# Performance work log

Measured on AMD Instinct MI355X. Metric: run time of the kernel, lower is better.

The kernel has to match this reference:

```python
import jax, jax.numpy as jnp
import numpy as np

N = 100000   # nodes
E = 1600000  # edges (avg degree 16)
D = 128      # in_channels == hidden_channels
H = 4        # heads
C = D // H   # per-head channels = 32


def leaky(x, slope):
    return jnp.where(x >= 0, x, slope * x)


def setup_inputs() -> dict:
    key = jax.random.key(0)
    ks = jax.random.split(key, 12)
    s = 1.0 / np.sqrt(D)
    return {
        "x": jax.random.normal(ks[0], (N, D), jnp.float32),
        "edge_index": jax.random.randint(ks[1], (2, E), 0, N, jnp.int32),
        "edge_type": jax.random.randint(ks[2], (E,), 0, 8, jnp.int32),
        # linear1 (first_layer=True): LeakyReLU(0.01) -> Linear(D, D)
        "W1": jax.random.normal(ks[3], (D, D), jnp.float32) * s,
        "b1": jnp.zeros((D,), jnp.float32),
        # GATConv params: lin (no bias), att_src/att_dst [1,H,C], output bias [H*C]
        "Wg": jax.random.normal(ks[4], (D, D), jnp.float32) * s,
        "att_src": jax.random.normal(ks[5], (1, H, C), jnp.float32) * s,
        "att_dst": jax.random.normal(ks[6], (1, H, C), jnp.float32) * s,
        "bias_g": jnp.zeros((D,), jnp.float32),
        # linear2: LeakyReLU(0.01) -> Linear(D, D)
        "W2": jax.random.normal(ks[7], (D, D), jnp.float32) * s,
        "b2": jnp.zeros((D,), jnp.float32),
    }


def reference(x, edge_index, edge_type, W1, b1, Wg, att_src, att_dst, bias_g, W2, b2):
    # dropout layers act in eval mode (identity); edge_type is unused by forward.
    # linear1: LeakyReLU(0.01) then Linear
    x = leaky(x, 0.01) @ W1.T + b1                      # [N, D]

    # GATConv (add_self_loops=False, concat heads)
    h = (x @ Wg.T).reshape(N, H, C)                     # [N, H, C]
    a_src = jnp.sum(h * att_src, axis=-1)               # [N, H]
    a_dst = jnp.sum(h * att_dst, axis=-1)               # [N, H]

    src, dst = edge_index[0], edge_index[1]
    alpha = leaky(a_src[src] + a_dst[dst], 0.2)          # [E, H]

    # segment softmax over destination nodes (numerically stable)
    amax = jax.ops.segment_max(alpha, dst, num_segments=N)   # [N, H], -inf for empty
    amax = jnp.where(jnp.isfinite(amax), amax, 0.0)
    ex = jnp.exp(alpha - amax[dst])                      # [E, H]
    denom = jax.ops.segment_sum(ex, dst, num_segments=N) # [N, H]
    coeff = ex / (denom[dst] + 1e-16)                    # [E, H]

    msg = h[src] * coeff[:, :, None]                     # [E, H, C]
    out = jax.ops.segment_sum(msg, dst, num_segments=N)  # [N, H, C]
    out = out.reshape(N, H * C) + bias_g                 # [N, D]

    # linear2: LeakyReLU(0.01) then Linear; Dropout(0.3) identity at eval
    out = leaky(out, 0.01) @ W2.T + b2                   # [N, D]
    return out
```

## Files before the change

### kernel.cpp

```cpp
#include <hip/hip_runtime.h>
#include <hip/hip_bf16.h>

#define D128 128

typedef __attribute__((ext_vector_type(8))) short bf16x8;
typedef __attribute__((ext_vector_type(4))) float f32x4;

__device__ __forceinline__ float b2f(unsigned short u) {
    union { unsigned int i; float f; } z;
    z.i = ((unsigned int)u) << 16;
    return z.f;
}

__device__ __forceinline__ unsigned short f2b(float f) {
    union { float f; unsigned int i; } z;
    z.f = f;
    unsigned int r = z.i + 0x7FFFu + ((z.i >> 16) & 1u);
    return (unsigned short)(r >> 16);
}

__device__ __forceinline__ f32x4 mfma16(bf16x8 a, bf16x8 b, f32x4 c) {
    return __builtin_amdgcn_mfma_f32_16x16x32_bf16(a, b, c, 0, 0, 0);
}

#define CHUNK 8192
#define MAXBINS 512
#define BINCAP 8192
#define NGB 768
#define NFB 768

__global__ __launch_bounds__(256) void k_prep1(
    const float* __restrict__ W1, const float* __restrict__ Wg,
    const float* __restrict__ b1,
    const int* __restrict__ ei, int* __restrict__ M,
    float* __restrict__ Wc, float* __restrict__ bc,
    int E, int B, int nbins)
{
    __shared__ float wgr[256];
    __shared__ int hist[MAXBINS];
    const int t = threadIdx.x;
    if (blockIdx.x < 64) {
        const int i0 = blockIdx.x * 2;
        wgr[t] = Wg[i0 * 128 + t];
        __syncthreads();
        const int half = t >> 7;
        const int j = t & 127;
        const float* wr = &wgr[half * 128];
        float acc = 0.f;
        #pragma unroll 4
        for (int k = 0; k < 128; ++k)
            acc += wr[k] * W1[k * 128 + j];
        Wc[(i0 + half) * 128 + j] = acc;
        if (j == 0) {
            float ab = 0.f;
            for (int k = 0; k < 128; ++k) ab += wr[k] * b1[k];
            bc[i0 + half] = ab;
        }
    } else {
        const int chunk = blockIdx.x - 64;
        for (int i = t; i < nbins; i += 256) hist[i] = 0;
        __syncthreads();
        const int base = chunk * CHUNK;
        const int end = min(base + CHUNK, E);
        for (int e = base + t; e < end; e += 256)
            atomicAdd(&hist[ei[E + e] >> 8], 1);
        __syncthreads();
        for (int i = t; i < nbins; i += 256)
            M[i * B + chunk] = hist[i];
    }
}

__global__ __launch_bounds__(256) void k_prep2s(
    const float* __restrict__ Wc, const float* __restrict__ bc,
    const float* __restrict__ att_s, const float* __restrict__ att_d,
    const float* __restrict__ W2,
    unsigned short* __restrict__ Wcat, unsigned short* __restrict__ W2l,
    float* __restrict__ lbias,
    const int* __restrict__ M, int* __restrict__ scanned,
    int* __restrict__ bsum, int nM)
{
    __shared__ int lds[256];
    const int b = blockIdx.x, t = threadIdx.x;
    if (b < 9) {
        const int q = b * 256 + t;
        const int ct = q >> 8, rem = q & 255;
        const int ks = rem >> 6, lane = rem & 63;
        const int ldiv = lane >> 4, lmod = lane & 15;
        const int kb = ks * 32 + ldiv * 8;
        float v[8];
        if (ct < 8) {
            const int rho = ct * 16 + lmod;
            const float4 a = *(const float4*)(Wc + rho * 128 + kb);
            const float4 bq = *(const float4*)(Wc + rho * 128 + kb + 4);
            v[0] = a.x; v[1] = a.y; v[2] = a.z; v[3] = a.w;
            v[4] = bq.x; v[5] = bq.y; v[6] = bq.z; v[7] = bq.w;
        } else {
            #pragma unroll
            for (int e = 0; e < 8; ++e) v[e] = 0.f;
            if (lmod < 8) {
                const int hh = lmod & 3;
                const float* av = lmod < 4 ? att_s : att_d;
                for (int c = 0; c < 32; ++c) {
                    const float w = av[hh * 32 + c];
                    const float* wrow = Wc + (hh * 32 + c) * 128 + kb;
                    #pragma unroll
                    for (int e = 0; e < 8; ++e) v[e] += w * wrow[e];
                }
            }
        }
        union { uint4 qq; unsigned short s[8]; } o;
        #pragma unroll
        for (int e = 0; e < 8; ++e) o.s[e] = f2b(v[e]);
        *(uint4*)(Wcat + q * 8) = o.qq;
    } else if (b < 17) {
        const int q = (b - 9) * 256 + t;
        const int ct = q >> 8, rem = q & 255;
        const int ks = rem >> 6, lane = rem & 63;
        const int ldiv = lane >> 4, lmod = lane & 15;
        const int kb = ks * 32 + ldiv * 8;
        const int rho = ct * 16 + lmod;
        const float4 a = *(const float4*)(W2 + rho * 128 + kb);
        const float4 bq = *(const float4*)(W2 + rho * 128 + kb + 4);
        union { uint4 qq; unsigned short s[8]; } o;
        o.s[0] = f2b(a.x); o.s[1] = f2b(a.y); o.s[2] = f2b(a.z); o.s[3] = f2b(a.w);
        o.s[4] = f2b(bq.x); o.s[5] = f2b(bq.y); o.s[6] = f2b(bq.z); o.s[7] = f2b(bq.w);
        *(uint4*)(W2l + q * 8) = o.qq;
    } else if (b == 17) {
        if (t < 144) {
            float v = 0.f;
            if (t < 128) v = bc[t];
            else if (t < 136) {
                const int hh = (t - 128) & 3;
                const float* av = t < 132 ? att_s : att_d;
                for (int c = 0; c < 32; ++c) v += av[hh * 32 + c] * bc[hh * 32 + c];
            }
            lbias[t] = v;
        }
    } else {
        const int sid = b - 18;
        const int g0 = sid * 1024 + t * 4;
        int v0 = g0     < nM ? M[g0]     : 0;
        int v1 = g0 + 1 < nM ? M[g0 + 1] : 0;
        int v2 = g0 + 2 < nM ? M[g0 + 2] : 0;
        int v3 = g0 + 3 < nM ? M[g0 + 3] : 0;
        const int s = v0 + v1 + v2 + v3;
        lds[t] = s;
        __syncthreads();
        #pragma unroll
        for (int off = 1; off < 256; off <<= 1) {
            int tv = t >= off ? lds[t - off] : 0;
            __syncthreads();
            lds[t] += tv;
            __syncthreads();
        }
        int run = lds[t] - s;
        if (g0     < nM) scanned[g0]     = run;
        run += v0;
        if (g0 + 1 < nM) scanned[g0 + 1] = run;
        run += v1;
        if (g0 + 2 < nM) scanned[g0 + 2] = run;
        run += v2;
        if (g0 + 3 < nM) scanned[g0 + 3] = run;
        if (t == 255) bsum[sid] = lds[255];
    }
}

__global__ __launch_bounds__(256) void k_gemmA2(
    const float* __restrict__ x,
    const unsigned short* __restrict__ Wcat,
    const float* __restrict__ lbias,
    unsigned short* __restrict__ hfeat,
    float* __restrict__ asrc, float* __restrict__ adst,
    const int* __restrict__ ei, const int* __restrict__ scanned,
    const int* __restrict__ bsum, unsigned int* __restrict__ binned,
    int N, int E, int B, int nbins, int nM, int ntiles)
{
    __shared__ __align__(16) unsigned char smem[36864];
    const int t = threadIdx.x;
    if (blockIdx.x >= B) {
        unsigned short* sW = (unsigned short*)smem;
        const int wave = t >> 6, lane = t & 63, lmod = lane & 15, ldiv = lane >> 4;

        #pragma unroll
        for (int r = 0; r < 9; ++r)
            *(uint4*)&sW[r * 2048 + t * 8] = *(const uint4*)(Wcat + r * 2048 + t * 8);
        __syncthreads();

        for (int tile = blockIdx.x - B; tile < ntiles; tile += NGB) {
            const int rowBase = tile * 64;
            int row = rowBase + wave * 16 + lmod;
            row = min(row, N - 1);
            bf16x8 afr[4];
            #pragma unroll
            for (int ks = 0; ks < 4; ++ks) {
                const float* px = x + (size_t)row * D128 + ks * 32 + ldiv * 8;
                float4 f0 = *(const float4*)px;
                float4 f1 = *(const float4*)(px + 4);
                float tmp[8] = { f0.x, f0.y, f0.z, f0.w, f1.x, f1.y, f1.z, f1.w };
                union { bf16x8 v; unsigned short s[8]; } o;
                #pragma unroll
                for (int jj = 0; jj < 8; ++jj) {
                    float f = tmp[jj];
                    f = f >= 0.f ? f : 0.01f * f;
                    o.s[jj] = f2b(f);
                }
                afr[ks] = o.v;
            }

            f32x4 acc[9] = {};
            #pragma unroll
            for (int ct = 0; ct < 9; ++ct) {
                #pragma unroll
                for (int ks = 0; ks < 4; ++ks) {
                    bf16x8 bfr = *(const bf16x8*)&sW[(ct * 256 + ks * 64 + lane) * 8];
                    acc[ct] = mfma16(afr[ks], bfr, acc[ct]);
                }
            }

            const int orow = rowBase + wave * 16 + ldiv * 4;
            #pragma unroll
            for (int ct = 0; ct < 8; ++ct) {
                const int col = ct * 16 + lmod;
                const float bias = lbias[col];
                #pragma unroll
                for (int r = 0; r < 4; ++r)
                    if (orow + r < N)
                        hfeat[(size_t)(orow + r) * D128 + col] = f2b(acc[ct][r] + bias);
            }
            if (lmod < 8) {
                const float lb = lbias[128 + lmod];
                float* dst = lmod < 4 ? asrc : adst;
                const int hh = lmod & 3;
                #pragma unroll
                for (int r = 0; r < 4; ++r)
                    if (orow + r < N)
                        dst[(size_t)(orow + r) * 4 + hh] = acc[8][r] + lb;
            }
        }
    } else {
        int* cursor = (int*)smem;
        int* bpre   = (int*)(smem + MAXBINS * 4);
        const int chunk = blockIdx.x;
        const int nsb = (nM + 1023) >> 10;
        for (int i = t; i < nsb; i += 256) bpre[i] = bsum[i];
        __syncthreads();
        if (t == 0) {
            int run = 0;
            for (int i = 0; i < nsb; ++i) { int tv = bpre[i]; bpre[i] = run; run += tv; }
        }
        __syncthreads();
        for (int i = t; i < nbins; i += 256) {
            const int idx = i * B + chunk;
            cursor[i] = scanned[idx] + bpre[idx >> 10];
        }
        __syncthreads();
        const int base = chunk * CHUNK;
        const int end = min(base + CHUNK, E);
        for (int e = base + t; e < end; e += 256) {
            const int s = ei[e], d = ei[E + e];
            const int pos = atomicAdd(&cursor[d >> 8], 1);
            binned[pos] = ((unsigned int)(d & 255) << 20) | (unsigned int)s;
        }
    }
}

__global__ __launch_bounds__(256) void kB(
    const unsigned int* __restrict__ binned, const int* __restrict__ scanned,
    const int* __restrict__ bsum, int* __restrict__ bucket,
    int* __restrict__ rowstart, int* __restrict__ rowend,
    int E, int B, int nbins, int N, int nM)
{
    __shared__ unsigned int eb[BINCAP];
    __shared__ int ldeg[256];
    __shared__ int lscan[256];
    __shared__ int lcur[256];
    __shared__ int bpre[1024];
    const int nsb = (nM + 1023) >> 10;
    for (int i = threadIdx.x; i < nsb; i += 256) bpre[i] = bsum[i];
    __syncthreads();
    if (threadIdx.x == 0) {
        int run = 0;
        for (int i = 0; i < nsb; ++i) { int tv = bpre[i]; bpre[i] = run; run += tv; }
    }
    __syncthreads();
    const int bin = blockIdx.x;
    const int i0 = bin * B;
    const int binstart = scanned[i0] + bpre[i0 >> 10];
    int binend;
    if (bin + 1 < nbins) {
        const int i1 = (bin + 1) * B;
        binend = scanned[i1] + bpre[i1 >> 10];
    } else {
        binend = E;
    }
    int n = binend - binstart;
    if (n > BINCAP) n = BINCAP;

    for (int i = threadIdx.x; i < n; i += 256) eb[i] = binned[binstart + i];
    ldeg[threadIdx.x] = 0;
    __syncthreads();
    for (int i = threadIdx.x; i < n; i += 256)
        atomicAdd(&ldeg[eb[i] >> 20], 1);
    __syncthreads();
    const int v = ldeg[threadIdx.x];
    lscan[threadIdx.x] = v;
    __syncthreads();
    #pragma unroll
    for (int off = 1; off < 256; off <<= 1) {
        int tv = threadIdx.x >= off ? lscan[threadIdx.x - off] : 0;
        __syncthreads();
        lscan[threadIdx.x] += tv;
        __syncthreads();
    }
    const int excl = lscan[threadIdx.x] - v;
    lcur[threadIdx.x] = excl;
    const int d = (bin << 8) + threadIdx.x;
    if (d < N) {
        rowstart[d] = binstart + excl;
        rowend[d]   = binstart + excl + v;
    }
    __syncthreads();
    for (int i = threadIdx.x; i < n; i += 256) {
        const unsigned int p = eb[i];
        const int lp = atomicAdd(&lcur[p >> 20], 1);
        bucket[binstart + lp] = (int)(p & 0xFFFFFu);
    }
}

__global__ __launch_bounds__(256) void k_gat(
    const int* __restrict__ bucket,
    const int* __restrict__ rowstart, const int* __restrict__ rowend,
    const float* __restrict__ asrc, const float* __restrict__ adst,
    const unsigned short* __restrict__ hfeat,
    const float* __restrict__ bias_g,
    unsigned short* __restrict__ outbf, int N)
{
    const int wave = threadIdx.x >> 6;
    const int lane = threadIdx.x & 63;
    const int g    = lane >> 4;
    const int gl   = lane & 15;
    const int h    = gl >> 2;
    const int d    = blockIdx.x * 16 + wave * 4 + g;

    int start = 0, end = 0;
    float a_d = 0.f;
    if (d < N) {
        start = rowstart[d];
        end   = rowend[d];
        a_d   = adst[(size_t)d * 4 + h];
    }
    const unsigned int chb = (unsigned int)(gl << 3);
    const unsigned short* hbase = hfeat + chb;

    float acc[8] = {0.f, 0.f, 0.f, 0.f, 0.f, 0.f, 0.f, 0.f};
    float denom = 0.f;

    int j = start;
    for (; j + 2 <= end; j += 2) {
        const int s0 = bucket[j];
        const int s1 = bucket[j + 1];
        const float as0 = asrc[((size_t)s0 << 2) + h];
        const float as1 = asrc[((size_t)s1 << 2) + h];
        const uint4 hp0 = *(const uint4*)(hbase + ((unsigned int)s0 << 7));
        const uint4 hp1 = *(const uint4*)(hbase + ((unsigned int)s1 << 7));
        float a0 = as0 + a_d; a0 = a0 >= 0.f ? a0 : 0.2f * a0;
        float a1 = as1 + a_d; a1 = a1 >= 0.f ? a1 : 0.2f * a1;
        const float w0 = __expf(a0), w1 = __expf(a1);
        denom += w0 + w1;
        acc[0] += w0 * b2f((unsigned short)(hp0.x & 0xFFFFu)) + w1 * b2f((unsigned short)(hp1.x & 0xFFFFu));
        acc[1] += w0 * b2f((unsigned short)(hp0.x >> 16))     + w1 * b2f((unsigned short)(hp1.x >> 16));
        acc[2] += w0 * b2f((unsigned short)(hp0.y & 0xFFFFu)) + w1 * b2f((unsigned short)(hp1.y & 0xFFFFu));
        acc[3] += w0 * b2f((unsigned short)(hp0.y >> 16))     + w1 * b2f((unsigned short)(hp1.y >> 16));
        acc[4] += w0 * b2f((unsigned short)(hp0.z & 0xFFFFu)) + w1 * b2f((unsigned short)(hp1.z & 0xFFFFu));
        acc[5] += w0 * b2f((unsigned short)(hp0.z >> 16))     + w1 * b2f((unsigned short)(hp1.z >> 16));
        acc[6] += w0 * b2f((unsigned short)(hp0.w & 0xFFFFu)) + w1 * b2f((unsigned short)(hp1.w & 0xFFFFu));
        acc[7] += w0 * b2f((unsigned short)(hp0.w >> 16))     + w1 * b2f((unsigned short)(hp1.w >> 16));
    }
    if (j < end) {
        const int s0 = bucket[j];
        const float as0 = asrc[((size_t)s0 << 2) + h];
        const uint4 hp0 = *(const uint4*)(hbase + ((unsigned int)s0 << 7));
        float a0 = as0 + a_d; a0 = a0 >= 0.f ? a0 : 0.2f * a0;
        const float w0 = __expf(a0);
        denom += w0;
        acc[0] += w0 * b2f((unsigned short)(hp0.x & 0xFFFFu));
        acc[1] += w0 * b2f((unsigned short)(hp0.x >> 16));
        acc[2] += w0 * b2f((unsigned short)(hp0.y & 0xFFFFu));
        acc[3] += w0 * b2f((unsigned short)(hp0.y >> 16));
        acc[4] += w0 * b2f((unsigned short)(hp0.z & 0xFFFFu));
        acc[5] += w0 * b2f((unsigned short)(hp0.z >> 16));
        acc[6] += w0 * b2f((unsigned short)(hp0.w & 0xFFFFu));
        acc[7] += w0 * b2f((unsigned short)(hp0.w >> 16));
    }

    if (d < N) {
        const float inv = 1.f / (denom + 1e-16f);
        const float4 bg0 = *(const float4*)(bias_g + chb);
        const float4 bg1 = *(const float4*)(bias_g + chb + 4);
        const float bg[8] = { bg0.x, bg0.y, bg0.z, bg0.w, bg1.x, bg1.y, bg1.z, bg1.w };
        unsigned short s[8];
        #pragma unroll
        for (int k2 = 0; k2 < 8; ++k2) {
            float v = acc[k2] * inv + bg[k2];
            v = v >= 0.f ? v : 0.01f * v;
            s[k2] = f2b(v);
        }
        uint4 o;
        o.x = ((unsigned int)s[1] << 16) | s[0];
        o.y = ((unsigned int)s[3] << 16) | s[2];
        o.z = ((unsigned int)s[5] << 16) | s[4];
        o.w = ((unsigned int)s[7] << 16) | s[6];
        *(uint4*)(outbf + (((unsigned int)d << 7) + chb)) = o;
    }
}

__global__ __launch_bounds__(256) void k_final(
    const unsigned short* __restrict__ gatbf,
    const unsigned short* __restrict__ W2l,
    const float* __restrict__ b2,
    float* __restrict__ out, int N, int ntiles)
{
    __shared__ __align__(16) unsigned short sW[16384];
    const int t = threadIdx.x;
    const int wave = t >> 6, lane = t & 63, lmod = lane & 15, ldiv = lane >> 4;

    #pragma unroll
    for (int r = 0; r < 8; ++r)
        *(uint4*)&sW[r * 2048 + t * 8] = *(const uint4*)(W2l + r * 2048 + t * 8);
    __syncthreads();

    for (int tile = blockIdx.x; tile < ntiles; tile += NFB) {
        const int rowBase = tile * 64;
        int row = rowBase + wave * 16 + lmod;
        row = min(row, N - 1);
        bf16x8 afr[4];
        #pragma unroll
        for (int ks = 0; ks < 4; ++ks)
            afr[ks] = *(const bf16x8*)(gatbf + (size_t)row * D128 + ks * 32 + ldiv * 8);

        f32x4 acc[8] = {};
        #pragma unroll
        for (int ct = 0; ct < 8; ++ct) {
            #pragma unroll
            for (int ks = 0; ks < 4; ++ks) {
                bf16x8 bfr = *(const bf16x8*)&sW[(ct * 256 + ks * 64 + lane) * 8];
                acc[ct] = mfma16(afr[ks], bfr, acc[ct]);
            }
        }

        const int orow = rowBase + wave * 16 + ldiv * 4;
        #pragma unroll
        for (int ct = 0; ct < 8; ++ct) {
            const int col = ct * 16 + lmod;
            const float bb = b2[col];
            #pragma unroll
            for (int r = 0; r < 4; ++r)
                if (orow + r < N)
                    out[(size_t)(orow + r) * D128 + col] = acc[ct][r] + bb;
        }
    }
}

extern "C" void kernel_launch(void* const* d_in, const int* in_sizes, int n_in,
                              void* d_out, int out_size, void* d_ws, size_t ws_size,
                              hipStream_t stream)
{
    const float* x    = (const float*)d_in[0];
    const int*   ei   = (const int*)d_in[1];
    const float* W1   = (const float*)d_in[3];
    const float* b1   = (const float*)d_in[4];
    const float* Wg   = (const float*)d_in[5];
    const float* atts = (const float*)d_in[6];
    const float* attd = (const float*)d_in[7];
    const float* bg   = (const float*)d_in[8];
    const float* W2   = (const float*)d_in[9];
    const float* b2   = (const float*)d_in[10];
    float* out = (float*)d_out;

    const int N = in_sizes[0] / D128;
    const int E = in_sizes[1] / 2;

    const int B     = (E + CHUNK - 1) / CHUNK;
    const int nbins = (N + 255) >> 8;
    const int nM    = nbins * B;
    const int nsb   = (nM + 1023) / 1024;
    const int ntiles = (N + 63) / 64;

    char* ws = (char*)d_ws;
    float* Wc = (float*)ws;
    size_t off = 65536;
    float* bc    = (float*)(ws + off); off += 512;
    float* lbias = (float*)(ws + off); off += 1024;
    unsigned short* Wcat = (unsigned short*)(ws + off); off += 36864;
    unsigned short* W2l  = (unsigned short*)(ws + off); off += 32768;
    unsigned short* hfeat = (unsigned short*)(ws + off); off += (size_t)N * D128 * 2;
    float* asrc = (float*)(ws + off); off += (size_t)N * 4 * 4;
    float* adst = (float*)(ws + off); off += (size_t)N * 4 * 4;
    int* M       = (int*)(ws + off); off += (size_t)nM * 4;
    int* scanned = (int*)(ws + off); off += (size_t)nM * 4;
    int* bsum    = (int*)(ws + off); off += 1024 * 4;
    unsigned int* binned = (unsigned int*)(ws + off); off += (size_t)E * 4;
    int* bucket  = (int*)(ws + off); off += (size_t)E * 4;
    int* rowstart = (int*)(ws + off); off += (size_t)N * 4;
    int* rowend   = (int*)(ws + off); off += (size_t)N * 4;
    unsigned short* outbf = (unsigned short*)(ws + off); off += (size_t)N * D128 * 2;

    k_prep1<<<64 + B, 256, 0, stream>>>(W1, Wg, b1, ei, M, Wc, bc, E, B, nbins);
    k_prep2s<<<18 + nsb, 256, 0, stream>>>(Wc, bc, atts, attd, W2, Wcat, W2l,
                                           lbias, M, scanned, bsum, nM);
    k_gemmA2<<<B + NGB, 256, 0, stream>>>(x, Wcat, lbias, hfeat, asrc, adst,
                                          ei, scanned, bsum, binned,
                                          N, E, B, nbins, nM, ntiles);
    kB<<<nbins, 256, 0, stream>>>(binned, scanned, bsum, bucket,
                                  rowstart, rowend, E, B, nbins, N, nM);
    k_gat<<<(N + 15) / 16, 256, 0, stream>>>(bucket, rowstart, rowend,
                                             asrc, adst, hfeat, bg, outbf, N);
    k_final<<<NFB, 256, 0, stream>>>(outbf, W2l, b2, out, N, ntiles);
}
```

Measured before the change: 275.3 us.

## Replace global scan-based edge binning with atomic fixed-capacity bins and fewer launches

```diff
diff --git a/kernel.cpp b/kernel.cpp
--- a/kernel.cpp
+++ b/kernel.cpp
@@ -23,25 +23,43 @@
     return __builtin_amdgcn_mfma_f32_16x16x32_bf16(a, b, c, 0, 0, 0);
 }
 
-#define CHUNK 8192
-#define MAXBINS 512
-#define BINCAP 8192
+#define CHUNK2 4096
+#define BINW   128
+#define BINCAP 4096
+#define MAXBINS 1024
 #define NGB 768
 #define NFB 768
 
-__global__ __launch_bounds__(256) void k_prep1(
+__global__ __launch_bounds__(256) void k_prep(
     const float* __restrict__ W1, const float* __restrict__ Wg,
     const float* __restrict__ b1,
-    const int* __restrict__ ei, int* __restrict__ M,
-    float* __restrict__ Wc, float* __restrict__ bc,
+    const float* __restrict__ att_s, const float* __restrict__ att_d,
+    const float* __restrict__ W2,
+    const int* __restrict__ ei,
+    unsigned short* __restrict__ Wcat, unsigned short* __restrict__ W2l,
+    float* __restrict__ lbias,
+    unsigned int* __restrict__ binned, int* __restrict__ binFill,
     int E, int B, int nbins)
 {
-    __shared__ float wgr[256];
-    __shared__ int hist[MAXBINS];
     const int t = threadIdx.x;
-    if (blockIdx.x < 64) {
-        const int i0 = blockIdx.x * 2;
-        wgr[t] = Wg[i0 * 128 + t];
+    const int b = blockIdx.x;
+    if (b < 68) {
+        __shared__ float wgr[256];
+        __shared__ float rowout[2][128];
+        if (b < 64) {
+            const int i0 = b * 2;
+            wgr[t] = Wg[i0 * 128 + t];
+        } else {
+            const int q = (b - 64) * 2 + (t >> 7);
+            const int h = q & 3;
+            const float* av = q < 4 ? att_s : att_d;
+            const int k = t & 127;
+            float v = 0.f;
+            #pragma unroll 8
+            for (int c = 0; c < 32; ++c)
+                v += av[h * 32 + c] * Wg[(h * 32 + c) * 128 + k];
+            wgr[t] = v;
+        }
         __syncthreads();
         const int half = t >> 7;
         const int j = t & 127;
@@ -50,70 +68,29 @@
         #pragma unroll 4
         for (int k = 0; k < 128; ++k)
             acc += wr[k] * W1[k * 128 + j];
-        Wc[(i0 + half) * 128 + j] = acc;
+        rowout[half][j] = acc;
         if (j == 0) {
             float ab = 0.f;
             for (int k = 0; k < 128; ++k) ab += wr[k] * b1[k];
-            bc[i0 + half] = ab;
-        }
-    } else {
-        const int chunk = blockIdx.x - 64;
-        for (int i = t; i < nbins; i += 256) hist[i] = 0;
-        __syncthreads();
-        const int base = chunk * CHUNK;
-        const int end = min(base + CHUNK, E);
-        for (int e = base + t; e < end; e += 256)
-            atomicAdd(&hist[ei[E + e] >> 8], 1);
-        __syncthreads();
-        for (int i = t; i < nbins; i += 256)
-            M[i * B + chunk] = hist[i];
-    }
-}
-
-__global__ __launch_bounds__(256) void k_prep2s(
-    const float* __restrict__ Wc, const float* __restrict__ bc,
-    const float* __restrict__ att_s, const float* __restrict__ att_d,
-    const float* __restrict__ W2,
-    unsigned short* __restrict__ Wcat, unsigned short* __restrict__ W2l,
-    float* __restrict__ lbias,
-    const int* __restrict__ M, int* __restrict__ scanned,
-    int* __restrict__ bsum, int nM)
-{
-    __shared__ int lds[256];
-    const int b = blockIdx.x, t = threadIdx.x;
-    if (b < 9) {
-        const int q = b * 256 + t;
-        const int ct = q >> 8, rem = q & 255;
-        const int ks = rem >> 6, lane = rem & 63;
-        const int ldiv = lane >> 4, lmod = lane & 15;
-        const int kb = ks * 32 + ldiv * 8;
-        float v[8];
-        if (ct < 8) {
-            const int rho = ct * 16 + lmod;
-            const float4 a = *(const float4*)(Wc + rho * 128 + kb);
-            const float4 bq = *(const float4*)(Wc + rho * 128 + kb + 4);
-            v[0] = a.x; v[1] = a.y; v[2] = a.z; v[3] = a.w;
-            v[4] = bq.x; v[5] = bq.y; v[6] = bq.z; v[7] = bq.w;
-        } else {
-            #pragma unroll
-            for (int e = 0; e < 8; ++e) v[e] = 0.f;
-            if (lmod < 8) {
-                const int hh = lmod & 3;
-                const float* av = lmod < 4 ? att_s : att_d;
-                for (int c = 0; c < 32; ++c) {
-                    const float w = av[hh * 32 + c];
-                    const float* wrow = Wc + (hh * 32 + c) * 128 + kb;
-                    #pragma unroll
-                    for (int e = 0; e < 8; ++e) v[e] += w * wrow[e];
-                }
-            }
-        }
-        union { uint4 qq; unsigned short s[8]; } o;
-        #pragma unroll
-        for (int e = 0; e < 8; ++e) o.s[e] = f2b(v[e]);
-        *(uint4*)(Wcat + q * 8) = o.qq;
-    } else if (b < 17) {
-        const int q = (b - 9) * 256 + t;
+            const int rho = (b < 64) ? b * 2 + half : 128 + (b - 64) * 2 + half;
+            lbias[rho] = ab;
+        }
+        __syncthreads();
+        if (t < 32) {
+            const int half2 = t >> 4;
+            const int rho = (b < 64) ? b * 2 + half2 : 128 + (b - 64) * 2 + half2;
+            const int idx16 = t & 15;
+            const int ks = idx16 >> 2, ldiv = idx16 & 3;
+            const int colb = ks * 32 + ldiv * 8;
+            const int ct = rho >> 4, lmod = rho & 15;
+            const int frag = (ct * 4 + ks) * 64 + ldiv * 16 + lmod;
+            union { uint4 q4; unsigned short s[8]; } o;
+            #pragma unroll
+            for (int e = 0; e < 8; ++e) o.s[e] = f2b(rowout[half2][colb + e]);
+            *(uint4*)(Wcat + frag * 8) = o.q4;
+        }
+    } else if (b < 76) {
+        const int q = (b - 68) * 256 + t;
         const int ct = q >> 8, rem = q & 255;
         const int ks = rem >> 6, lane = rem & 63;
         const int ldiv = lane >> 4, lmod = lane & 15;
@@ -125,59 +102,86 @@
         o.s[0] = f2b(a.x); o.s[1] = f2b(a.y); o.s[2] = f2b(a.z); o.s[3] = f2b(a.w);
         o.s[4] = f2b(bq.x); o.s[5] = f2b(bq.y); o.s[6] = f2b(bq.z); o.s[7] = f2b(bq.w);
         *(uint4*)(W2l + q * 8) = o.qq;
-    } else if (b == 17) {
-        if (t < 144) {
-            float v = 0.f;
-            if (t < 128) v = bc[t];
-            else if (t < 136) {
-                const int hh = (t - 128) & 3;
-                const float* av = t < 132 ? att_s : att_d;
-                for (int c = 0; c < 32; ++c) v += av[hh * 32 + c] * bc[hh * 32 + c];
-            }
-            lbias[t] = v;
-        }
     } else {
-        const int sid = b - 18;
-        const int g0 = sid * 1024 + t * 4;
-        int v0 = g0     < nM ? M[g0]     : 0;
-        int v1 = g0 + 1 < nM ? M[g0 + 1] : 0;
-        int v2 = g0 + 2 < nM ? M[g0 + 2] : 0;
-        int v3 = g0 + 3 < nM ? M[g0 + 3] : 0;
-        const int s = v0 + v1 + v2 + v3;
-        lds[t] = s;
-        __syncthreads();
-        #pragma unroll
-        for (int off = 1; off < 256; off <<= 1) {
-            int tv = t >= off ? lds[t - off] : 0;
-            __syncthreads();
-            lds[t] += tv;
-            __syncthreads();
-        }
-        int run = lds[t] - s;
-        if (g0     < nM) scanned[g0]     = run;
-        run += v0;
-        if (g0 + 1 < nM) scanned[g0 + 1] = run;
-        run += v1;
-        if (g0 + 2 < nM) scanned[g0 + 2] = run;
-        run += v2;
-        if (g0 + 3 < nM) scanned[g0 + 3] = run;
-        if (t == 255) bsum[sid] = lds[255];
-    }
-}
-
-__global__ __launch_bounds__(256) void k_gemmA2(
+        __shared__ int hist[MAXBINS];
+        const int chunk = b - 76;
+        for (int i = t; i < nbins; i += 256) hist[i] = 0;
+        __syncthreads();
+        const int base = chunk * CHUNK2;
+        const int end = min(base + CHUNK2, E);
+        for (int e = base + t; e < end; e += 256)
+            atomicAdd(&hist[ei[E + e] >> 7], 1);
+        __syncthreads();
+        for (int i = t; i < nbins; i += 256) {
+            const int c = hist[i];
+            hist[i] = c > 0 ? atomicAdd(&binFill[i], c) : 0;
+        }
+        __syncthreads();
+        for (int e = base + t; e < end; e += 256) {
+            const int s = ei[e], d = ei[E + e];
+            const int bin = d >> 7;
+            const int pos = atomicAdd(&hist[bin], 1);
+            if (pos < BINCAP)
+                binned[(size_t)bin * BINCAP + pos] =
+                    ((unsigned int)(d & 127) << 20) | (unsigned int)s;
+        }
+    }
+}
+
+__global__ __launch_bounds__(256) void k_mid(
     const float* __restrict__ x,
     const unsigned short* __restrict__ Wcat,
     const float* __restrict__ lbias,
     unsigned short* __restrict__ hfeat,
     float* __restrict__ asrc, float* __restrict__ adst,
-    const int* __restrict__ ei, const int* __restrict__ scanned,
-    const int* __restrict__ bsum, unsigned int* __restrict__ binned,
-    int N, int E, int B, int nbins, int nM, int ntiles)
+    const unsigned int* __restrict__ binned, const int* __restrict__ binFill,
+    int* __restrict__ bucket,
+    int* __restrict__ rowstart, int* __restrict__ rowend,
+    int N, int nbins, int ntiles)
 {
     __shared__ __align__(16) unsigned char smem[36864];
     const int t = threadIdx.x;
-    if (blockIdx.x >= B) {
+    if (blockIdx.x < nbins) {
+        unsigned int* eb = (unsigned int*)smem;
+        int* ldeg  = (int*)(smem + 16384);
+        int* lscan = ldeg + 128;
+        int* lcur  = lscan + 128;
+        const int bin = blockIdx.x;
+        int n = binFill[bin];
+        if (n > BINCAP) n = BINCAP;
+        const int bb = bin * BINCAP;
+        for (int i = t; i < n; i += 256) eb[i] = binned[(size_t)bb + i];
+        if (t < 128) ldeg[t] = 0;
+        __syncthreads();
+        for (int i = t; i < n; i += 256)
+            atomicAdd(&ldeg[eb[i] >> 20], 1);
+        __syncthreads();
+        int v = 0;
+        if (t < 128) { v = ldeg[t]; lscan[t] = v; }
+        __syncthreads();
+        #pragma unroll
+        for (int off = 1; off < 128; off <<= 1) {
+            int tv = (t < 128 && t >= off) ? lscan[t - off] : 0;
+            __syncthreads();
+            if (t < 128) lscan[t] += tv;
+            __syncthreads();
+        }
+        if (t < 128) {
+            const int excl = lscan[t] - v;
+            lcur[t] = excl;
+            const int d = (bin << 7) + t;
+            if (d < N) {
+                rowstart[d] = bb + excl;
+                rowend[d]   = bb + excl + v;
+            }
+        }
+        __syncthreads();
+        for (int i = t; i < n; i += 256) {
+            const unsigned int p = eb[i];
+            const int lp = atomicAdd(&lcur[p >> 20], 1);
+            bucket[(size_t)bb + lp] = (int)(p & 0xFFFFFu);
+        }
+    } else {
         unsigned short* sW = (unsigned short*)smem;
         const int wave = t >> 6, lane = t & 63, lmod = lane & 15, ldiv = lane >> 4;
 
@@ -186,7 +190,7 @@
             *(uint4*)&sW[r * 2048 + t * 8] = *(const uint4*)(Wcat + r * 2048 + t * 8);
         __syncthreads();
 
-        for (int tile = blockIdx.x - B; tile < ntiles; tile += NGB) {
+        for (int tile = blockIdx.x - nbins; tile < ntiles; tile += NGB) {
             const int rowBase = tile * 64;
             int row = rowBase + wave * 16 + lmod;
             row = min(row, N - 1);
@@ -237,93 +241,6 @@
                         dst[(size_t)(orow + r) * 4 + hh] = acc[8][r] + lb;
             }
         }
-    } else {
-        int* cursor = (int*)smem;
-        int* bpre   = (int*)(smem + MAXBINS * 4);
-        const int chunk = blockIdx.x;
-        const int nsb = (nM + 1023) >> 10;
-        for (int i = t; i < nsb; i += 256) bpre[i] = bsum[i];
-        __syncthreads();
-        if (t == 0) {
-            int run = 0;
-            for (int i = 0; i < nsb; ++i) { int tv = bpre[i]; bpre[i] = run; run += tv; }
-        }
-        __syncthreads();
-        for (int i = t; i < nbins; i += 256) {
-            const int idx = i * B + chunk;
-            cursor[i] = scanned[idx] + bpre[idx >> 10];
-        }
-        __syncthreads();
-        const int base = chunk * CHUNK;
-        const int end = min(base + CHUNK, E);
-        for (int e = base + t; e < end; e += 256) {
-            const int s = ei[e], d = ei[E + e];
-            const int pos = atomicAdd(&cursor[d >> 8], 1);
-            binned[pos] = ((unsigned int)(d & 255) << 20) | (unsigned int)s;
-        }
-    }
-}
-
-__global__ __launch_bounds__(256) void kB(
-    const unsigned int* __restrict__ binned, const int* __restrict__ scanned,
-    const int* __restrict__ bsum, int* __restrict__ bucket,
-    int* __restrict__ rowstart, int* __restrict__ rowend,
-    int E, int B, int nbins, int N, int nM)
-{
-    __shared__ unsigned int eb[BINCAP];
-    __shared__ int ldeg[256];
-    __shared__ int lscan[256];
-    __shared__ int lcur[256];
-    __shared__ int bpre[1024];
-    const int nsb = (nM + 1023) >> 10;
-    for (int i = threadIdx.x; i < nsb; i += 256) bpre[i] = bsum[i];
-    __syncthreads();
-    if (threadIdx.x == 0) {
-        int run = 0;
-        for (int i = 0; i < nsb; ++i) { int tv = bpre[i]; bpre[i] = run; run += tv; }
-    }
-    __syncthreads();
-    const int bin = blockIdx.x;
-    const int i0 = bin * B;
-    const int binstart = scanned[i0] + bpre[i0 >> 10];
-    int binend;
-    if (bin + 1 < nbins) {
-        const int i1 = (bin + 1) * B;
-        binend = scanned[i1] + bpre[i1 >> 10];
-    } else {
-        binend = E;
-    }
-    int n = binend - binstart;
-    if (n > BINCAP) n = BINCAP;
-
-    for (int i = threadIdx.x; i < n; i += 256) eb[i] = binned[binstart + i];
-    ldeg[threadIdx.x] = 0;
-    __syncthreads();
-    for (int i = threadIdx.x; i < n; i += 256)
-        atomicAdd(&ldeg[eb[i] >> 20], 1);
-    __syncthreads();
-    const int v = ldeg[threadIdx.x];
-    lscan[threadIdx.x] = v;
-    __syncthreads();
-    #pragma unroll
-    for (int off = 1; off < 256; off <<= 1) {
-        int tv = threadIdx.x >= off ? lscan[threadIdx.x - off] : 0;
-        __syncthreads();
-        lscan[threadIdx.x] += tv;
-        __syncthreads();
-    }
-    const int excl = lscan[threadIdx.x] - v;
-    lcur[threadIdx.x] = excl;
-    const int d = (bin << 8) + threadIdx.x;
-    if (d < N) {
-        rowstart[d] = binstart + excl;
-        rowend[d]   = binstart + excl + v;
-    }
-    __syncthreads();
-    for (int i = threadIdx.x; i < n; i += 256) {
-        const unsigned int p = eb[i];
-        const int lp = atomicAdd(&lcur[p >> 20], 1);
-        bucket[binstart + lp] = (int)(p & 0xFFFFFu);
     }
 }
 
@@ -480,39 +397,34 @@
     const int N = in_sizes[0] / D128;
     const int E = in_sizes[1] / 2;
 
-    const int B     = (E + CHUNK - 1) / CHUNK;
-    const int nbins = (N + 255) >> 8;
-    const int nM    = nbins * B;
-    const int nsb   = (nM + 1023) / 1024;
+    const int B      = (E + CHUNK2 - 1) / CHUNK2;
+    const int nbins  = (N + BINW - 1) / BINW;
     const int ntiles = (N + 63) / 64;
 
     char* ws = (char*)d_ws;
-    float* Wc = (float*)ws;
-    size_t off = 65536;
-    float* bc    = (float*)(ws + off); off += 512;
-    float* lbias = (float*)(ws + off); off += 1024;
+    size_t off = 0;
     unsigned short* Wcat = (unsigned short*)(ws + off); off += 36864;
     unsigned short* W2l  = (unsigned short*)(ws + off); off += 32768;
+    float* lbias = (float*)(ws + off); off += 1024;
+    int* binFill = (int*)(ws + off); off += (size_t)((nbins * 4 + 15) & ~15);
     unsigned short* hfeat = (unsigned short*)(ws + off); off += (size_t)N * D128 * 2;
     float* asrc = (float*)(ws + off); off += (size_t)N * 4 * 4;
     float* adst = (float*)(ws + off); off += (size_t)N * 4 * 4;
-    int* M       = (int*)(ws + off); off += (size_t)nM * 4;
-    int* scanned = (int*)(ws + off); off += (size_t)nM * 4;
-    int* bsum    = (int*)(ws + off); off += 1024 * 4;
-    unsigned int* binned = (unsigned int*)(ws + off); off += (size_t)E * 4;
-    int* bucket  = (int*)(ws + off); off += (size_t)E * 4;
+    unsigned int* binned = (unsigned int*)(ws + off); off += (size_t)nbins * BINCAP * 4;
+    int* bucket  = (int*)(ws + off); off += (size_t)nbins * BINCAP * 4;
     int* rowstart = (int*)(ws + off); off += (size_t)N * 4;
     int* rowend   = (int*)(ws + off); off += (size_t)N * 4;
     unsigned short* outbf = (unsigned short*)(ws + off); off += (size_t)N * D128 * 2;
 
-    k_prep1<<<64 + B, 256, 0, stream>>>(W1, Wg, b1, ei, M, Wc, bc, E, B, nbins);
-    k_prep2s<<<18 + nsb, 256, 0, stream>>>(Wc, bc, atts, attd, W2, Wcat, W2l,
-                                           lbias, M, scanned, bsum, nM);
-    k_gemmA2<<<B + NGB, 256, 0, stream>>>(x, Wcat, lbias, hfeat, asrc, adst,
-                                          ei, scanned, bsum, binned,
-                                          N, E, B, nbins, nM, ntiles);
-    kB<<<nbins, 256, 0, stream>>>(binned, scanned, bsum, bucket,
-                                  rowstart, rowend, E, B, nbins, N, nM);
+    hipMemsetAsync(Wcat, 0, 36864, stream);
+    hipMemsetAsync(binFill, 0, (size_t)nbins * 4, stream);
+
+    k_prep<<<76 + B, 256, 0, stream>>>(W1, Wg, b1, atts, attd, W2, ei,
+                                       Wcat, W2l, lbias, binned, binFill,
+                                       E, B, nbins);
+    k_mid<<<nbins + NGB, 256, 0, stream>>>(x, Wcat, lbias, hfeat, asrc, adst,
+                                           binned, binFill, bucket,
+                                           rowstart, rowend, N, nbins, ntiles);
     k_gat<<<(N + 15) / 16, 256, 0, stream>>>(bucket, rowstart, rowend,
                                              asrc, adst, hfeat, bg, outbf, N);
     k_final<<<NFB, 256, 0, stream>>>(outbf, W2l, b2, out, N, ntiles);
```

Result: slower. 304.1 us (+10.5%).
